# Optimization experiments

Measured on AMD Instinct MI355X. Metric: run time of the kernel, lower is better.

The kernel has to match this reference:

```python
import jax, jax.numpy as jnp
import numpy as np

R = 6
P = 2 * R + 1          # 13, correlation patch size
N = P * P              # 169 displacements
C = 32                 # one-hot label channels
FOUR_LN2 = 4.0 * float(np.log(2.0))


def _extract_windows(x, h, w):
    """Zero-pad by R and extract all PxP shifted views.
    x: (b, c, h, w) -> (b, c, N, h, w), displacement index n = dy*P + dx,
    matching both SpatialCorrelationSampler patch ordering and F.unfold."""
    xp = jnp.pad(x, ((0, 0), (0, 0), (R, R), (R, R)))
    return jnp.stack([xp[:, :, dy:dy + h, dx:dx + w]
                      for dy in range(P) for dx in range(P)], axis=2)


def setup_inputs():
    key = jax.random.key(0)
    k1, k2, k3 = jax.random.split(key, 3)
    feats_r = jax.random.normal(k1, (2, 2, 128, 64, 64), dtype=jnp.float32)
    feats_t = jax.random.normal(k2, (2, 128, 64, 64), dtype=jnp.float32)
    quantized_r = jax.random.randint(k3, (2, 2, 1, 256, 256), 0, C)
    return {"feats_r": feats_r, "feats_t": feats_t, "quantized_r": quantized_r}


def reference(feats_r, feats_t, quantized_r):
    nref, b, c, h, w = feats_r.shape
    hw = h * w

    # ---- local PxP correlation volume per reference (SpatialCorrelationSampler, k=1) ----
    corrs = []
    for i in range(nref):
        win = _extract_windows(feats_r[i], h, w)                       # (b,c,N,h,w)
        corrs.append(jnp.einsum('bchw,bcnhw->bnhw', feats_t, win).reshape(b, N, hw))
    corr = jax.nn.softmax(jnp.concatenate(corrs, axis=1), axis=1)      # (b, nref*N, hw)

    # ---- compact_verify: top-2 + gaussian heatmap refinement ----
    cc = corr.reshape(b, nref, N, hw).transpose(0, 1, 3, 2).reshape(b, nref * hw, N)
    ccd = jax.lax.stop_gradient(cc)                                     # torch uses .detach()
    vals, idx = jax.lax.top_k(ccd, 2)                                   # (b, L, 2)
    wts = jax.nn.softmax(vals, axis=-1)
    ys = (idx // P).astype(jnp.float32)
    xs = (idx % P).astype(jnp.float32)
    grid = jnp.arange(P, dtype=jnp.float32)
    dx = grid[None, None, None, :] - xs[..., None]                      # (b,L,2,P)
    dy = grid[None, None, None, :] - ys[..., None]                      # (b,L,2,P)
    heat = jnp.exp(-FOUR_LN2 * (dx[:, :, :, None, :] ** 2 + dy[:, :, :, :, None] ** 2))  # (b,L,2,P,P) [yy,xx]
    corr_heat = jnp.einsum('blkn,blk->bln', heat.reshape(b, nref * hw, 2, N), wts)
    vmax = jnp.max(vals, axis=-1, keepdims=True)
    corr2 = jnp.where(vmax > 0.1, corr_heat, cc)                        # mask/refine
    corr2 = corr2.reshape(b, nref, hw, N).transpose(0, 1, 3, 2).reshape(b, nref * N, hw)

    # ---- get_out: unfold one-hot reference labels and weighted-sum over window ----
    scale = quantized_r.shape[-2] // h                                  # prep: stride subsample
    ufs = []
    for i in range(nref):
        lab = quantized_r[i, :, 0, ::scale, ::scale]                    # (b,h,w)
        oh = jnp.transpose(jax.nn.one_hot(lab, C, dtype=feats_t.dtype), (0, 3, 1, 2))
        ufs.append(_extract_windows(oh, h, w).reshape(b, C, N, hw))
    image_uf = jnp.concatenate(ufs, axis=2)                             # (b,C,nref*N,hw)
    image_uf = image_uf.at[:, 1:].multiply(1.15)                        # inference boost
    out = jnp.einsum('bnl,bcnl->bcl', corr2, image_uf)
    return out.reshape(b, C, h, w)
```

## Files before the change

### kernel.cpp

```cpp
#include <hip/hip_runtime.h>
#include <math.h>

namespace {

constexpr int RAD  = 6;
constexpr int P    = 13;
constexpr int NWIN = 169;
constexpr int NTOT = 338;
constexpr int NCH  = 128;
constexpr int NCLS = 32;
constexpr int W    = 64;
constexpr int HW   = 4096;
constexpr float FOUR_LN2 = 2.772588722239781f;

constexpr int TX    = 32;
constexpr int CHUNK = 8;
constexpr int PW    = 48;
constexpr int PR    = 13;
constexpr int FRELEMS = CHUNK * PR * PW;
constexpr int NCHUNK  = NCH / CHUNK;
constexpr int TILE    = TX * NWIN;

__device__ __forceinline__ bool better(float va, int ia, float vb, int ib) {
  return (va > vb) || ((va == vb) && (ia < ib));
}

__global__ __launch_bounds__(256, 2) void corr_kernel(
    const float* __restrict__ fr,
    const float* __restrict__ ft,
    float* __restrict__ vol) {
  const int blk = blockIdx.x;
  const int xh = blk & 1;
  const int y  = (blk >> 1) & 63;
  const int bi = blk >> 7;
  const int b  = bi >> 1;
  const int ii = bi & 1;
  const int x0 = xh * TX;
  const int t  = threadIdx.x;
  const int cg = t >> 7;
  const int tl = t & 127;

  __shared__ __align__(16) float smem[2 * FRELEMS];
  __shared__ __align__(16) float ftbuf[2][CHUNK * TX];

  const int xg = tl & 7;
  const int dy = tl >> 3;
  const bool comp = (tl < 104);

  const float* frbase = fr + (size_t)((ii * 2 + b) * NCH) * HW;
  const float* ftp = ft + (size_t)(b * NCH + (t >> 5)) * HW + y * W + x0 + (t & 31);

  int offc[20];
  unsigned vmsk = 0u;
  #pragma unroll
  for (int u = 0; u < 20; ++u) {
    const int e = t + u * 256;
    int o = 0;
    if (e < FRELEMS) {
      const int cc  = e / (PR * PW);
      const int rem = e - cc * (PR * PW);
      const int r   = rem / PW;
      const int xc  = rem - r * PW;
      const int yy  = y + r - RAD;
      const int xx  = x0 - RAD + xc;
      if ((unsigned)yy < 64u && (unsigned)xx < 64u && xc < 44) {
        o = cc * HW + yy * W + xx;
        vmsk |= (1u << u);
      }
    }
    offc[u] = o;
  }

  float acc[13][4];
  #pragma unroll
  for (int dx = 0; dx < 13; ++dx)
    #pragma unroll
    for (int k = 0; k < 4; ++k) acc[dx][k] = 0.f;

  float rg[20];
  float rft;

  auto stage_load = [&](int c0) {
    const float* fb = frbase + (size_t)c0 * HW;
    #pragma unroll
    for (int u = 0; u < 20; ++u) {
      const float v = fb[offc[u]];
      rg[u] = (vmsk & (1u << u)) ? v : 0.f;
    }
    rft = ftp[(size_t)c0 * HW];
  };
  auto stage_write = [&](int s) {
    float* frb = smem + s * FRELEMS;
    #pragma unroll
    for (int u = 0; u < 20; ++u) {
      const int e = t + u * 256;
      if (e < FRELEMS) frb[e] = rg[u];
    }
    ftbuf[s][t] = rft;
  };

  stage_load(0);
  stage_write(0);
  __syncthreads();

  for (int k = 0; k < NCHUNK; ++k) {
    const int cur = k & 1;
    if (k < NCHUNK - 1) stage_load((k + 1) * CHUNK);
    if (comp) {
      const float* frb = smem + cur * FRELEMS;
      #pragma unroll
      for (int c2 = 0; c2 < 4; ++c2) {
        const int cc = cg * 4 + c2;
        const float* fp = frb + (cc * PR + dy) * PW + xg * 4;
        float w[16];
        #pragma unroll
        for (int j = 0; j < 4; ++j) {
          const float4 q4 = *(const float4*)(fp + 4 * j);
          w[4 * j] = q4.x; w[4 * j + 1] = q4.y; w[4 * j + 2] = q4.z; w[4 * j + 3] = q4.w;
        }
        const float4 tq = *(const float4*)(&ftbuf[cur][cc * TX + xg * 4]);
        const float tqa[4] = {tq.x, tq.y, tq.z, tq.w};
        #pragma unroll
        for (int dx = 0; dx < 13; ++dx)
          #pragma unroll
          for (int kk = 0; kk < 4; ++kk)
            acc[dx][kk] = fmaf(w[dx + kk], tqa[kk], acc[dx][kk]);
      }
    }
    __syncthreads();
    if (k < NCHUNK - 1) stage_write(cur ^ 1);
    __syncthreads();
  }

  if (comp && cg == 1) {
    float* rb = smem + tl * 52;
    #pragma unroll
    for (int dx = 0; dx < 13; ++dx)
      *(float4*)(rb + dx * 4) = make_float4(acc[dx][0], acc[dx][1], acc[dx][2], acc[dx][3]);
  }
  __syncthreads();
  if (comp && cg == 0) {
    const float* rb = smem + tl * 52;
    #pragma unroll
    for (int dx = 0; dx < 13; ++dx) {
      const float4 r = *(const float4*)(rb + dx * 4);
      acc[dx][0] += r.x; acc[dx][1] += r.y; acc[dx][2] += r.z; acc[dx][3] += r.w;
    }
  }
  __syncthreads();
  if (comp && cg == 0) {
    #pragma unroll
    for (int dx = 0; dx < 13; ++dx)
      #pragma unroll
      for (int kk = 0; kk < 4; ++kk)
        smem[(xg * 4 + kk) * NWIN + dy * 13 + dx] = acc[dx][kk];
  }
  __syncthreads();
  {
    float* gb = vol + ((size_t)(b * HW + y * W + x0) * 2 + ii) * NWIN;
    for (int u = 0; u < 22; ++u) {
      const int e = t + u * 256;
      if (e < TILE) {
        const int xl2 = e / NWIN;
        const int mm  = e - xl2 * NWIN;
        gb[(size_t)xl2 * (2 * NWIN) + mm] = smem[e];
      }
    }
  }
}

__global__ __launch_bounds__(256) void lab_kernel(
    const int* __restrict__ q, int* __restrict__ lab) {
  const int idx = blockIdx.x * 256 + threadIdx.x;
  const int i2b = idx >> 12;
  const int rem = idx & 4095;
  const int yy  = rem >> 6;
  const int xx  = rem & 63;
  lab[idx] = q[(size_t)i2b * 65536 + (yy * 4) * 256 + xx * 4];
}

__global__ __launch_bounds__(256) void post_kernel(
    const float* __restrict__ vol,
    const int*  __restrict__ lab,
    float* __restrict__ out) {
  const int blk  = blockIdx.x;
  const int t    = threadIdx.x;
  const int w    = t >> 6;
  const int lane = t & 63;
  const int pix  = blk * 4 + w;
  const int b = pix >> 12;
  const int y = (pix >> 6) & 63;
  const int x = pix & 63;

  __shared__ float accS[4][NCLS];
  accS[w][lane & 31] = 0.f;

  float vv[6];
  float lmax = -INFINITY;
  const float* vp = vol + (size_t)pix * NTOT;
  #pragma unroll
  for (int k = 0; k < 6; ++k) {
    const int e = lane + 64 * k;
    vv[k] = (e < NTOT) ? vp[e] : -INFINITY;
    lmax = fmaxf(lmax, vv[k]);
  }
  #pragma unroll
  for (int off = 32; off > 0; off >>= 1)
    lmax = fmaxf(lmax, __shfl_xor(lmax, off));

  float p[6];
  float lsum = 0.f;
  #pragma unroll
  for (int k = 0; k < 6; ++k) {
    const int e = lane + 64 * k;
    p[k] = (e < NTOT) ? __expf(vv[k] - lmax) : 0.f;
    lsum += p[k];
  }
  #pragma unroll
  for (int off = 32; off > 0; off >>= 1)
    lsum += __shfl_xor(lsum, off);
  const float rinv = 1.f / lsum;
  #pragma unroll
  for (int k = 0; k < 6; ++k) p[k] *= rinv;

  float a1_0 = -1.f, a2_0 = -1.f, a1_1 = -1.f, a2_1 = -1.f;
  int   j1_0 = 1 << 20, j2_0 = 1 << 20, j1_1 = 1 << 20, j2_1 = 1 << 20;
  #pragma unroll
  for (int k = 0; k < 6; ++k) {
    const int e = lane + 64 * k;
    if (e < NTOT) {
      const int r = (e >= NWIN) ? 1 : 0;
      const int m = e - r * NWIN;
      const float pv = p[k];
      if (r == 0) {
        if (better(pv, m, a1_0, j1_0)) { a2_0 = a1_0; j2_0 = j1_0; a1_0 = pv; j1_0 = m; }
        else if (better(pv, m, a2_0, j2_0)) { a2_0 = pv; j2_0 = m; }
      } else {
        if (better(pv, m, a1_1, j1_1)) { a2_1 = a1_1; j2_1 = j1_1; a1_1 = pv; j1_1 = m; }
        else if (better(pv, m, a2_1, j2_1)) { a2_1 = pv; j2_1 = m; }
      }
    }
  }
  #pragma unroll
  for (int off = 32; off > 0; off >>= 1) {
    {
      const float u1 = __shfl_xor(a1_0, off); const int q1 = __shfl_xor(j1_0, off);
      const float u2 = __shfl_xor(a2_0, off); const int q2 = __shfl_xor(j2_0, off);
      if (better(u1, q1, a1_0, j1_0)) {
        float nv2; int ni2;
        if (better(a1_0, j1_0, u2, q2)) { nv2 = a1_0; ni2 = j1_0; }
        else                            { nv2 = u2;   ni2 = q2; }
        a1_0 = u1; j1_0 = q1; a2_0 = nv2; j2_0 = ni2;
      } else if (better(u1, q1, a2_0, j2_0)) { a2_0 = u1; j2_0 = q1; }
    }
    {
      const float u1 = __shfl_xor(a1_1, off); const int q1 = __shfl_xor(j1_1, off);
      const float u2 = __shfl_xor(a2_1, off); const int q2 = __shfl_xor(j2_1, off);
      if (better(u1, q1, a1_1, j1_1)) {
        float nv2; int ni2;
        if (better(a1_1, j1_1, u2, q2)) { nv2 = a1_1; ni2 = j1_1; }
        else                            { nv2 = u2;   ni2 = q2; }
        a1_1 = u1; j1_1 = q1; a2_1 = nv2; j2_1 = ni2;
      } else if (better(u1, q1, a2_1, j2_1)) { a2_1 = u1; j2_1 = q1; }
    }
  }

  const float e10 = __expf(a1_0), e20 = __expf(a2_0);
  const float rs0 = 1.f / (e10 + e20);
  const float w00 = e10 * rs0, w10 = e20 * rs0;
  const bool  fl0 = (a1_0 > 0.1f);
  const float xs00 = (float)(j1_0 % P), ys00 = (float)(j1_0 / P);
  const float xs10 = (float)(j2_0 % P), ys10 = (float)(j2_0 / P);

  const float e11 = __expf(a1_1), e21 = __expf(a2_1);
  const float rs1 = 1.f / (e11 + e21);
  const float w01 = e11 * rs1, w11 = e21 * rs1;
  const bool  fl1 = (a1_1 > 0.1f);
  const float xs01 = (float)(j1_1 % P), ys01 = (float)(j1_1 / P);
  const float xs11 = (float)(j2_1 % P), ys11 = (float)(j2_1 / P);

  #pragma unroll
  for (int k = 0; k < 6; ++k) {
    const int e = lane + 64 * k;
    if (e < NTOT) {
      const int r  = (e >= NWIN) ? 1 : 0;
      const int m  = e - r * NWIN;
      const int dy = m / P;
      const int dx = m - dy * P;
      const bool  fl = r ? fl1 : fl0;
      float val;
      if (fl) {
        const float wA = r ? w01 : w00, wB = r ? w11 : w10;
        const float xA = r ? xs01 : xs00, yA = r ? ys01 : ys00;
        const float xB = r ? xs11 : xs10, yB = r ? ys11 : ys10;
        const float fdx0 = (float)dx - xA, fdy0 = (float)dy - yA;
        const float fdx1 = (float)dx - xB, fdy1 = (float)dy - yB;
        val = wA * __expf(-FOUR_LN2 * (fdx0 * fdx0 + fdy0 * fdy0))
            + wB * __expf(-FOUR_LN2 * (fdx1 * fdx1 + fdy1 * fdy1));
      } else {
        val = p[k];
      }
      const int yy = y + dy - RAD;
      const int xx = x + dx - RAD;
      if ((unsigned)yy < 64u && (unsigned)xx < 64u) {
        const int cls = lab[(size_t)(r * 2 + b) * 4096 + yy * W + xx];
        atomicAdd(&accS[w][cls], val);
      }
    }
  }
  __syncthreads();

  if (t < 4 * NCLS) {
    const int cls = t >> 2;
    const int j   = t & 3;
    const int x0  = (blk * 4) & 63;
    const float sc = (cls == 0) ? 1.0f : 1.15f;
    out[(size_t)(b * NCLS + cls) * HW + y * W + x0 + j] = accS[j][cls] * sc;
  }
}

}

extern "C" void kernel_launch(void* const* d_in, const int* in_sizes, int n_in,
                              void* d_out, int out_size, void* d_ws, size_t ws_size,
                              hipStream_t stream) {
  const float* fr = (const float*)d_in[0];
  const float* ft = (const float*)d_in[1];
  const int*   q  = (const int*)d_in[2];
  float* out = (float*)d_out;
  float* vol = (float*)d_ws;
  int*   lab = (int*)((char*)d_ws + (size_t)2 * HW * NTOT * sizeof(float));

  lab_kernel<<<dim3(64), dim3(256), 0, stream>>>(q, lab);
  corr_kernel<<<dim3(2 * 2 * 64 * 2), dim3(256), 0, stream>>>(fr, ft, vol);
  post_kernel<<<dim3(2 * HW / 4), dim3(256), 0, stream>>>(vol, lab, out);
}
```

Measured before the change: 60.88 us.

## Split correlation channel reduction across two blocks and sum partials in post kernel

The correlation kernel now splits the 128 feature channels into two halves handled by separate blocks, doubling the grid, and writes two partial volumes that the post kernel adds on load. It also narrows the shared-memory row pitch from 48 to 44 to cut per-block LDS, packs the gather offsets into 16-bit pairs to save registers, raises launch bounds to 4 blocks per CU, and drops one barrier per chunk iteration. The intent is more occupancy and parallelism on a grid that was too small. The cost is an extra partial-volume write and read, and the removed barrier could let the next stage's shared-memory write race with reads of the current buffer. That part looks safe because the two double buffers alternate, but it is risky.

Result: slower. 140.8 us (+131.3%).

```diff
diff --git a/kernel.cpp b/kernel.cpp
--- a/kernel.cpp
+++ b/kernel.cpp
@@ -15,24 +15,28 @@
 
 constexpr int TX    = 32;
 constexpr int CHUNK = 8;
-constexpr int PW    = 48;
+constexpr int BCH   = 64;
+constexpr int NCHUNK2 = BCH / CHUNK;
+constexpr int PW    = 44;
 constexpr int PR    = 13;
 constexpr int FRELEMS = CHUNK * PR * PW;
-constexpr int NCHUNK  = NCH / CHUNK;
-constexpr int TILE    = TX * NWIN;
+constexpr int NLD   = 18;
+constexpr int TILE  = TX * NWIN;
+constexpr size_t VOLH = (size_t)2 * HW * NTOT;
 
 __device__ __forceinline__ bool better(float va, int ia, float vb, int ib) {
   return (va > vb) || ((va == vb) && (ia < ib));
 }
 
-__global__ __launch_bounds__(256, 2) void corr_kernel(
+__global__ __launch_bounds__(256, 4) void corr_kernel(
     const float* __restrict__ fr,
     const float* __restrict__ ft,
     float* __restrict__ vol) {
   const int blk = blockIdx.x;
-  const int xh = blk & 1;
-  const int y  = (blk >> 1) & 63;
-  const int bi = blk >> 7;
+  const int h  = blk & 1;
+  const int xh = (blk >> 1) & 1;
+  const int y  = (blk >> 2) & 63;
+  const int bi = blk >> 8;
   const int b  = bi >> 1;
   const int ii = bi & 1;
   const int x0 = xh * TX;
@@ -47,15 +51,15 @@
   const int dy = tl >> 3;
   const bool comp = (tl < 104);
 
-  const float* frbase = fr + (size_t)((ii * 2 + b) * NCH) * HW;
-  const float* ftp = ft + (size_t)(b * NCH + (t >> 5)) * HW + y * W + x0 + (t & 31);
-
-  int offc[20];
+  const float* frbase = fr + (size_t)((ii * 2 + b) * NCH + h * BCH) * HW;
+  const float* ftp = ft + (size_t)(b * NCH + h * BCH + (t >> 5)) * HW + y * W + x0 + (t & 31);
+
+  unsigned offp[9];
   unsigned vmsk = 0u;
   #pragma unroll
-  for (int u = 0; u < 20; ++u) {
+  for (int u = 0; u < NLD; ++u) {
     const int e = t + u * 256;
-    int o = 0;
+    unsigned o = 0;
     if (e < FRELEMS) {
       const int cc  = e / (PR * PW);
       const int rem = e - cc * (PR * PW);
@@ -63,12 +67,12 @@
       const int xc  = rem - r * PW;
       const int yy  = y + r - RAD;
       const int xx  = x0 - RAD + xc;
-      if ((unsigned)yy < 64u && (unsigned)xx < 64u && xc < 44) {
-        o = cc * HW + yy * W + xx;
+      if ((unsigned)yy < 64u && (unsigned)xx < 64u) {
+        o = (unsigned)(cc * HW + yy * W + xx);
         vmsk |= (1u << u);
       }
     }
-    offc[u] = o;
+    if (u & 1) offp[u >> 1] |= (o << 16); else offp[u >> 1] = o;
   }
 
   float acc[13][4];
@@ -77,14 +81,15 @@
     #pragma unroll
     for (int k = 0; k < 4; ++k) acc[dx][k] = 0.f;
 
-  float rg[20];
+  float rg[NLD];
   float rft;
 
   auto stage_load = [&](int c0) {
     const float* fb = frbase + (size_t)c0 * HW;
     #pragma unroll
-    for (int u = 0; u < 20; ++u) {
-      const float v = fb[offc[u]];
+    for (int u = 0; u < NLD; ++u) {
+      const int o = (u & 1) ? (int)(offp[u >> 1] >> 16) : (int)(offp[u >> 1] & 0xffffu);
+      const float v = fb[o];
       rg[u] = (vmsk & (1u << u)) ? v : 0.f;
     }
     rft = ftp[(size_t)c0 * HW];
@@ -92,7 +97,7 @@
   auto stage_write = [&](int s) {
     float* frb = smem + s * FRELEMS;
     #pragma unroll
-    for (int u = 0; u < 20; ++u) {
+    for (int u = 0; u < NLD; ++u) {
       const int e = t + u * 256;
       if (e < FRELEMS) frb[e] = rg[u];
     }
@@ -103,9 +108,9 @@
   stage_write(0);
   __syncthreads();
 
-  for (int k = 0; k < NCHUNK; ++k) {
+  for (int k = 0; k < NCHUNK2; ++k) {
     const int cur = k & 1;
-    if (k < NCHUNK - 1) stage_load((k + 1) * CHUNK);
+    if (k < NCHUNK2 - 1) stage_load((k + 1) * CHUNK);
     if (comp) {
       const float* frb = smem + cur * FRELEMS;
       #pragma unroll
@@ -127,8 +132,7 @@
             acc[dx][kk] = fmaf(w[dx + kk], tqa[kk], acc[dx][kk]);
       }
     }
-    __syncthreads();
-    if (k < NCHUNK - 1) stage_write(cur ^ 1);
+    if (k < NCHUNK2 - 1) stage_write(cur ^ 1);
     __syncthreads();
   }
 
@@ -157,7 +161,7 @@
   }
   __syncthreads();
   {
-    float* gb = vol + ((size_t)(b * HW + y * W + x0) * 2 + ii) * NWIN;
+    float* gb = vol + (size_t)h * VOLH + ((size_t)(b * HW + y * W + x0) * 2 + ii) * NWIN;
     for (int u = 0; u < 22; ++u) {
       const int e = t + u * 256;
       if (e < TILE) {
@@ -201,7 +205,7 @@
   #pragma unroll
   for (int k = 0; k < 6; ++k) {
     const int e = lane + 64 * k;
-    vv[k] = (e < NTOT) ? vp[e] : -INFINITY;
+    vv[k] = (e < NTOT) ? (vp[e] + vp[VOLH + e]) : -INFINITY;
     lmax = fmaxf(lmax, vv[k]);
   }
   #pragma unroll
@@ -329,9 +333,9 @@
   const int*   q  = (const int*)d_in[2];
   float* out = (float*)d_out;
   float* vol = (float*)d_ws;
-  int*   lab = (int*)((char*)d_ws + (size_t)2 * HW * NTOT * sizeof(float));
+  int*   lab = (int*)((char*)d_ws + 2 * VOLH * sizeof(float));
 
   lab_kernel<<<dim3(64), dim3(256), 0, stream>>>(q, lab);
-  corr_kernel<<<dim3(2 * 2 * 64 * 2), dim3(256), 0, stream>>>(fr, ft, vol);
+  corr_kernel<<<dim3(2 * 2 * 64 * 2 * 2), dim3(256), 0, stream>>>(fr, ft, vol);
   post_kernel<<<dim3(2 * HW / 4), dim3(256), 0, stream>>>(vol, lab, out);
 }
```

## Stage correlation tiles with direct global-to-LDS loads instead of register staging

Applied to the files above, without the earlier changes.

The double-buffered staging of reference and target feature chunks now uses async global-to-LDS loads instead of loading into registers and then writing to shared memory. Out-of-bounds padding lanes read from a small zeroed scratch page, which the label kernel clears, and per-lane global pointers advance each chunk. This removes the staging registers, the separate LDS write pass and one barrier per chunk iteration. The cost is that correctness depends on the compiler inserting the right vmcnt waits before the barrier, and the change adds scratch-buffer plumbing.

Result: slower. 66.27 us (+8.9%).

```diff
diff --git a/kernel.cpp b/kernel.cpp
--- a/kernel.cpp
+++ b/kernel.cpp
@@ -18,8 +18,13 @@
 constexpr int PW    = 48;
 constexpr int PR    = 13;
 constexpr int FRELEMS = CHUNK * PR * PW;
-constexpr int NCHUNK  = NCH / CHUNK;
-constexpr int TILE    = TX * NWIN;
+constexpr int NLD   = 20;
+constexpr int NCHUNK = NCH / CHUNK;
+constexpr int TILE  = TX * NWIN;
+constexpr size_t VOLF = (size_t)2 * HW * NTOT;
+
+typedef const __attribute__((address_space(1))) void* gas_t;
+typedef __attribute__((address_space(3))) void*       las_t;
 
 __device__ __forceinline__ bool better(float va, int ia, float vb, int ib) {
   return (va > vb) || ((va == vb) && (ia < ib));
@@ -28,7 +33,8 @@
 __global__ __launch_bounds__(256, 2) void corr_kernel(
     const float* __restrict__ fr,
     const float* __restrict__ ft,
-    float* __restrict__ vol) {
+    float* __restrict__ vol,
+    const float* __restrict__ zp) {
   const int blk = blockIdx.x;
   const int xh = blk & 1;
   const int y  = (blk >> 1) & 63;
@@ -50,12 +56,12 @@
   const float* frbase = fr + (size_t)((ii * 2 + b) * NCH) * HW;
   const float* ftp = ft + (size_t)(b * NCH + (t >> 5)) * HW + y * W + x0 + (t & 31);
 
-  int offc[20];
+  const float* ga[NLD];
   unsigned vmsk = 0u;
   #pragma unroll
-  for (int u = 0; u < 20; ++u) {
+  for (int u = 0; u < NLD; ++u) {
     const int e = t + u * 256;
-    int o = 0;
+    const float* a = zp;
     if (e < FRELEMS) {
       const int cc  = e / (PR * PW);
       const int rem = e - cc * (PR * PW);
@@ -64,11 +70,11 @@
       const int yy  = y + r - RAD;
       const int xx  = x0 - RAD + xc;
       if ((unsigned)yy < 64u && (unsigned)xx < 64u && xc < 44) {
-        o = cc * HW + yy * W + xx;
+        a = frbase + cc * HW + yy * W + xx;
         vmsk |= (1u << u);
       }
     }
-    offc[u] = o;
+    ga[u] = a;
   }
 
   float acc[13][4];
@@ -77,35 +83,34 @@
     #pragma unroll
     for (int k = 0; k < 4; ++k) acc[dx][k] = 0.f;
 
-  float rg[20];
-  float rft;
-
-  auto stage_load = [&](int c0) {
-    const float* fb = frbase + (size_t)c0 * HW;
-    #pragma unroll
-    for (int u = 0; u < 20; ++u) {
-      const float v = fb[offc[u]];
-      rg[u] = (vmsk & (1u << u)) ? v : 0.f;
-    }
-    rft = ftp[(size_t)c0 * HW];
+  auto stage_issue = [&](int s) {
+    float* frb = smem + s * FRELEMS;
+    #pragma unroll
+    for (int u = 0; u < NLD; ++u) {
+      const int e = t + u * 256;
+      if (e < FRELEMS) {
+        __builtin_amdgcn_global_load_lds((gas_t)ga[u], (las_t)(frb + e), 4, 0, 0);
+      }
+    }
+    __builtin_amdgcn_global_load_lds((gas_t)ftp, (las_t)(&ftbuf[s][t]), 4, 0, 0);
   };
-  auto stage_write = [&](int s) {
-    float* frb = smem + s * FRELEMS;
-    #pragma unroll
-    for (int u = 0; u < 20; ++u) {
-      const int e = t + u * 256;
-      if (e < FRELEMS) frb[e] = rg[u];
-    }
-    ftbuf[s][t] = rft;
+  auto stage_advance = [&]() {
+    #pragma unroll
+    for (int u = 0; u < NLD; ++u)
+      ga[u] += ((vmsk >> u) & 1u) ? (CHUNK * HW) : 0;
+    ftp += (size_t)CHUNK * HW;
   };
 
-  stage_load(0);
-  stage_write(0);
+  stage_issue(0);
+  stage_advance();
   __syncthreads();
 
   for (int k = 0; k < NCHUNK; ++k) {
     const int cur = k & 1;
-    if (k < NCHUNK - 1) stage_load((k + 1) * CHUNK);
+    if (k < NCHUNK - 1) {
+      stage_issue(cur ^ 1);
+      stage_advance();
+    }
     if (comp) {
       const float* frb = smem + cur * FRELEMS;
       #pragma unroll
@@ -128,8 +133,6 @@
       }
     }
     __syncthreads();
-    if (k < NCHUNK - 1) stage_write(cur ^ 1);
-    __syncthreads();
   }
 
   if (comp && cg == 1) {
@@ -170,13 +173,14 @@
 }
 
 __global__ __launch_bounds__(256) void lab_kernel(
-    const int* __restrict__ q, int* __restrict__ lab) {
+    const int* __restrict__ q, int* __restrict__ lab, float* __restrict__ zp) {
   const int idx = blockIdx.x * 256 + threadIdx.x;
   const int i2b = idx >> 12;
   const int rem = idx & 4095;
   const int yy  = rem >> 6;
   const int xx  = rem & 63;
   lab[idx] = q[(size_t)i2b * 65536 + (yy * 4) * 256 + xx * 4];
+  if (idx < 1024) zp[idx] = 0.f;
 }
 
 __global__ __launch_bounds__(256) void post_kernel(
@@ -329,9 +333,10 @@
   const int*   q  = (const int*)d_in[2];
   float* out = (float*)d_out;
   float* vol = (float*)d_ws;
-  int*   lab = (int*)((char*)d_ws + (size_t)2 * HW * NTOT * sizeof(float));
-
-  lab_kernel<<<dim3(64), dim3(256), 0, stream>>>(q, lab);
-  corr_kernel<<<dim3(2 * 2 * 64 * 2), dim3(256), 0, stream>>>(fr, ft, vol);
+  int*   lab = (int*)((char*)d_ws + VOLF * sizeof(float));
+  float* zp  = (float*)((char*)lab + 16384 * sizeof(int));
+
+  lab_kernel<<<dim3(64), dim3(256), 0, stream>>>(q, lab, zp);
+  corr_kernel<<<dim3(2 * 2 * 64 * 2), dim3(256), 0, stream>>>(fr, ft, vol, zp);
   post_kernel<<<dim3(2 * HW / 4), dim3(256), 0, stream>>>(vol, lab, out);
 }
```

## Prefetch feature chunks two stages ahead and drop redundant barrier in correlation loop

Applied to the files above, without the earlier changes.

The correlation kernel now keeps two register staging buffers, so global loads for chunk k+2 are issued while chunk k is computed and chunk k+1 is committed to shared memory. This gives load latency more time to hide. One of the two __syncthreads per iteration is removed, since the shared-memory double buffer only needs the barrier at the end of each iteration. The cost is about 20 extra live registers per thread under a 2-blocks-per-SM launch bound, which could raise register pressure or cause spills.

Result: slower. 78.37 us (+28.7%).

```diff
diff --git a/kernel.cpp b/kernel.cpp
--- a/kernel.cpp
+++ b/kernel.cpp
@@ -18,8 +18,10 @@
 constexpr int PW    = 48;
 constexpr int PR    = 13;
 constexpr int FRELEMS = CHUNK * PR * PW;
-constexpr int NCHUNK  = NCH / CHUNK;
-constexpr int TILE    = TX * NWIN;
+constexpr int NLD   = 20;
+constexpr int NCHUNK = NCH / CHUNK;
+constexpr int TILE  = TX * NWIN;
+constexpr size_t VOLF = (size_t)2 * HW * NTOT;
 
 __device__ __forceinline__ bool better(float va, int ia, float vb, int ib) {
   return (va > vb) || ((va == vb) && (ia < ib));
@@ -50,10 +52,10 @@
   const float* frbase = fr + (size_t)((ii * 2 + b) * NCH) * HW;
   const float* ftp = ft + (size_t)(b * NCH + (t >> 5)) * HW + y * W + x0 + (t & 31);
 
-  int offc[20];
+  int offc[NLD];
   unsigned vmsk = 0u;
   #pragma unroll
-  for (int u = 0; u < 20; ++u) {
+  for (int u = 0; u < NLD; ++u) {
     const int e = t + u * 256;
     int o = 0;
     if (e < FRELEMS) {
@@ -77,35 +79,39 @@
     #pragma unroll
     for (int k = 0; k < 4; ++k) acc[dx][k] = 0.f;
 
-  float rg[20];
-  float rft;
-
-  auto stage_load = [&](int c0) {
+  float rgA[NLD], rgB[NLD];
+  float rftA, rftB;
+
+  auto stage_load = [&](int c0, float (&rg)[NLD], float& rft) {
     const float* fb = frbase + (size_t)c0 * HW;
     #pragma unroll
-    for (int u = 0; u < 20; ++u) {
+    for (int u = 0; u < NLD; ++u) {
       const float v = fb[offc[u]];
       rg[u] = (vmsk & (1u << u)) ? v : 0.f;
     }
     rft = ftp[(size_t)c0 * HW];
   };
-  auto stage_write = [&](int s) {
+  auto stage_write = [&](int s, const float (&rg)[NLD], float rft) {
     float* frb = smem + s * FRELEMS;
     #pragma unroll
-    for (int u = 0; u < 20; ++u) {
+    for (int u = 0; u < NLD; ++u) {
       const int e = t + u * 256;
       if (e < FRELEMS) frb[e] = rg[u];
     }
     ftbuf[s][t] = rft;
   };
 
-  stage_load(0);
-  stage_write(0);
+  stage_load(0, rgA, rftA);
+  stage_write(0, rgA, rftA);
+  stage_load(CHUNK, rgB, rftB);
   __syncthreads();
 
   for (int k = 0; k < NCHUNK; ++k) {
     const int cur = k & 1;
-    if (k < NCHUNK - 1) stage_load((k + 1) * CHUNK);
+    if (k < NCHUNK - 2) {
+      if (k & 1) stage_load((k + 2) * CHUNK, rgB, rftB);
+      else       stage_load((k + 2) * CHUNK, rgA, rftA);
+    }
     if (comp) {
       const float* frb = smem + cur * FRELEMS;
       #pragma unroll
@@ -127,8 +133,10 @@
             acc[dx][kk] = fmaf(w[dx + kk], tqa[kk], acc[dx][kk]);
       }
     }
-    __syncthreads();
-    if (k < NCHUNK - 1) stage_write(cur ^ 1);
+    if (k < NCHUNK - 1) {
+      if (k & 1) stage_write(cur ^ 1, rgA, rftA);
+      else       stage_write(cur ^ 1, rgB, rftB);
+    }
     __syncthreads();
   }
 
@@ -329,7 +337,7 @@
   const int*   q  = (const int*)d_in[2];
   float* out = (float*)d_out;
   float* vol = (float*)d_ws;
-  int*   lab = (int*)((char*)d_ws + (size_t)2 * HW * NTOT * sizeof(float));
+  int*   lab = (int*)((char*)d_ws + VOLF * sizeof(float));
 
   lab_kernel<<<dim3(64), dim3(256), 0, stream>>>(q, lab);
   corr_kernel<<<dim3(2 * 2 * 64 * 2), dim3(256), 0, stream>>>(fr, ft, vol);
```
